# Performance work log

Hardware: AMD Instinct MI355X
Metric: run time of the kernel (lower is better)

The kernel has to match this reference:

```python
import jax, jax.numpy as jnp
import numpy as np

N = 50000      # nodes
E = 800000     # edges
F_IN = 128     # input_channels
H = 128        # hidden_channels
OUT = 10       # output_channels
G = 64         # graphs in batch


def setup_inputs() -> dict:
    key = jax.random.key(0)
    ks = jax.random.split(key, 16)
    s = 0.05
    inp = {
        "x": jax.random.normal(ks[0], (N, F_IN), jnp.float32),
        "edge_index": jax.random.randint(ks[1], (2, E), 0, N, jnp.int64 if jax.config.jax_enable_x64 else jnp.int32),
        "batch": jnp.sort(jax.random.randint(ks[2], (N,), 0, G, jnp.int32)),
        "conv1_w": jax.random.normal(ks[3], (F_IN, H), jnp.float32) * s,
        "conv1_b": jnp.zeros((H,), jnp.float32),
        "conv2_w": jax.random.normal(ks[4], (H, H), jnp.float32) * s,
        "conv2_b": jnp.zeros((H,), jnp.float32),
        "conv3_w": jax.random.normal(ks[5], (H, H), jnp.float32) * s,
        "conv3_b": jnp.zeros((H,), jnp.float32),
        "fc1_w": jax.random.normal(ks[6], (H, 8 * H), jnp.float32) * s,
        "fc1_b": jnp.zeros((8 * H,), jnp.float32),
        "fc2_w": jax.random.normal(ks[7], (8 * H, 4 * H), jnp.float32) * s,
        "fc2_b": jnp.zeros((4 * H,), jnp.float32),
        "fc3_w": jax.random.normal(ks[8], (4 * H, 2 * H), jnp.float32) * s,
        "fc3_b": jnp.zeros((2 * H,), jnp.float32),
        "fc4_w": jax.random.normal(ks[9], (2 * H, H), jnp.float32) * s,
        "fc4_b": jnp.zeros((H,), jnp.float32),
        "fc5_w": jax.random.normal(ks[10], (H, OUT), jnp.float32) * s,
        "fc5_b": jnp.zeros((OUT,), jnp.float32),
    }
    return inp


def _gcn_conv(x, w, b, src, dst, norm, n_nodes):
    # GCNConv: out = D^{-1/2} (A + I) D^{-1/2} X W + b   (self-loops already in src/dst)
    xw = x @ w                                        # [N, H]
    msg = xw[src] * norm[:, None]                     # gather + scale, [E+N, H]
    return jax.ops.segment_sum(msg, dst, num_segments=n_nodes) + b


def reference(x, edge_index, batch,
              conv1_w, conv1_b, conv2_w, conv2_b, conv3_w, conv3_b,
              fc1_w, fc1_b, fc2_w, fc2_b, fc3_w, fc3_b,
              fc4_w, fc4_b, fc5_w, fc5_b):
    n = x.shape[0]
    loop = jnp.arange(n, dtype=edge_index.dtype)
    src = jnp.concatenate([edge_index[0], loop])      # add self-loops
    dst = jnp.concatenate([edge_index[1], loop])
    deg = jax.ops.segment_sum(jnp.ones_like(dst, dtype=x.dtype), dst, num_segments=n)
    dinv = jnp.where(deg > 0, jax.lax.rsqrt(deg), 0.0)
    norm = dinv[src] * dinv[dst]                      # symmetric normalization per edge

    h = jax.nn.relu(_gcn_conv(x, conv1_w, conv1_b, src, dst, norm, n))
    h = jax.nn.relu(_gcn_conv(h, conv2_w, conv2_b, src, dst, norm, n))
    h = _gcn_conv(h, conv3_w, conv3_b, src, dst, norm, n)

    # global mean pool over graphs
    sums = jax.ops.segment_sum(h, batch, num_segments=G)
    cnt = jax.ops.segment_sum(jnp.ones((n,), x.dtype), batch, num_segments=G)
    f = sums / jnp.maximum(cnt, 1.0)[:, None]         # [G, H]

    y = jax.nn.relu(f @ fc1_w + fc1_b)
    y = jax.nn.relu(y @ fc2_w + fc2_b)
    y = jax.nn.relu(y @ fc3_w + fc3_b)
    y = jax.nn.relu(y @ fc4_w + fc4_b)
    # dropout p=0.5 is identity in eval mode
    y = y @ fc5_w + fc5_b                             # [G, OUT]
    return (f, y)
```

## Files before the change

### kernel.cpp

```cpp
#include <hip/hip_runtime.h>
#include <stdint.h>

#define N_NODES 50000
#define N_EDGES 800000
#define N_PAD   50176
#define PCHUNK  512
#define NCHUNKS 98
#define FEAT    128
#define NGRAPH  64

#define E_BLKS      3125
#define GSTRIP_BLKS 782
#define GR_BLKS     (GSTRIP_BLKS + E_BLKS)
#define CZ_BLKS     3136
#define CP_BLKS     1563
#define Z2_BLKS     65
#define PREP_BLKS   (32 + CZ_BLKS + CP_BLKS + Z2_BLKS)
#define E1_SPLIT    399872
#define AGGC_GRID   (1563 * 9)

typedef __attribute__((ext_vector_type(8))) short short8;
typedef __attribute__((ext_vector_type(4))) float floatx4;

static __device__ __forceinline__ ushort f2bf(float f) {
  uint32_t x = __float_as_uint(f);
  x += 0x7FFF + ((x >> 16) & 1);
  return (ushort)(x >> 16);
}
static __device__ __forceinline__ float bfLo(uint32_t u) {
  return __uint_as_float(u << 16);
}
static __device__ __forceinline__ float bfHi(uint32_t u) {
  return __uint_as_float(u & 0xFFFF0000u);
}

static __device__ __forceinline__ void cvt4T(const float* __restrict__ in,
                                             ushort* __restrict__ outT, int i) {
  float4 v = ((const float4*)in)[i];
  int k = (4 * i) >> 7;
  int n = (4 * i) & 127;
  outT[(size_t)(n + 0) * FEAT + k] = f2bf(v.x);
  outT[(size_t)(n + 1) * FEAT + k] = f2bf(v.y);
  outT[(size_t)(n + 2) * FEAT + k] = f2bf(v.z);
  outT[(size_t)(n + 3) * FEAT + k] = f2bf(v.w);
}

__global__ __launch_bounds__(256) void prep_fused(const float* __restrict__ w0,
                                                  const float* __restrict__ w1,
                                                  ushort* __restrict__ wbT,
                                                  float* __restrict__ coefT,
                                                  float4* __restrict__ zcnt,
                                                  float4* __restrict__ zfy) {
  int b = blockIdx.x, t = threadIdx.x;
  if (b < 32) {
    int i = b * 256 + t;
    if (i < 4096) cvt4T(w0, wbT, i);
    else cvt4T(w1, wbT + FEAT * FEAT, i - 4096);
  } else if (b < 32 + CZ_BLKS) {
    int i = (b - 32) * 256 + t;
    ((float4*)coefT)[i] = make_float4(0.f, 0.f, 0.f, 0.f);
  } else if (b < 32 + CZ_BLKS + CP_BLKS) {
    int i = (b - 32 - CZ_BLKS) * 256 + t;
    if (i < 400000) zcnt[i] = make_float4(0.f, 0.f, 0.f, 0.f);
  } else {
    int i = (b - 32 - CZ_BLKS - CP_BLKS) * 256 + t;
    if (i < 16400) zfy[i] = make_float4(0.f, 0.f, 0.f, 0.f);
  }
}

static __device__ __forceinline__ void gemm_strip_f32a(int strip, int lane,
                                                       const float* __restrict__ X,
                                                       const ushort* __restrict__ WT,
                                                       ushort* __restrict__ XW) {
  if (strip >= N_NODES / 16) return;
  int m0 = strip * 16;
  int r = lane & 15, quad = lane >> 4;
  const float* xrow = X + (size_t)(m0 + r) * FEAT;
  short8 afr[4];
#pragma unroll
  for (int kb = 0; kb < 4; ++kb) {
    int k0 = kb * 32 + quad * 8;
    float4 f0 = *(const float4*)(xrow + k0);
    float4 f1 = *(const float4*)(xrow + k0 + 4);
    short8 a;
    a[0] = (short)f2bf(f0.x); a[1] = (short)f2bf(f0.y);
    a[2] = (short)f2bf(f0.z); a[3] = (short)f2bf(f0.w);
    a[4] = (short)f2bf(f1.x); a[5] = (short)f2bf(f1.y);
    a[6] = (short)f2bf(f1.z); a[7] = (short)f2bf(f1.w);
    afr[kb] = a;
  }
#pragma unroll
  for (int nt = 0; nt < 8; ++nt) {
    int n0 = nt * 16;
    floatx4 acc = {0.f, 0.f, 0.f, 0.f};
    const ushort* wrow = WT + (size_t)(n0 + r) * FEAT;
#pragma unroll
    for (int kb = 0; kb < 4; ++kb) {
      short8 b = *(const short8*)(wrow + kb * 32 + quad * 8);
      acc = __builtin_amdgcn_mfma_f32_16x16x32_bf16(afr[kb], b, acc, 0, 0, 0);
    }
#pragma unroll
    for (int reg = 0; reg < 4; ++reg)
      XW[(size_t)(m0 + quad * 4 + reg) * FEAT + n0 + r] = f2bf(acc[reg]);
  }
}

__global__ __launch_bounds__(256) void gemm_rank(const float* __restrict__ x,
                                                 const ushort* __restrict__ wbT,
                                                 ushort* __restrict__ msl,
                                                 const int* __restrict__ dst,
                                                 int* __restrict__ cnt_p,
                                                 int* __restrict__ rank) {
  int b = blockIdx.x, t = threadIdx.x;
  int fifth = b / 5;
  if (b - fifth * 5 == 0) {
    gemm_strip_f32a(fifth * 4 + (t >> 6), t & 63, x, wbT, msl);
  } else {
    int e = (b - fifth - 1) * 256 + t;
    rank[e] = atomicAdd(&cnt_p[dst[e] * 32], 1);
  }
}

__global__ __launch_bounds__(256) void gemm2_strip(const ushort* __restrict__ X,
                                                   const ushort* __restrict__ WT,
                                                   ushort* __restrict__ XW) {
  int strip = (blockIdx.x * 256 + threadIdx.x) >> 6;
  int lane = threadIdx.x & 63;
  if (strip >= N_NODES / 16) return;
  int m0 = strip * 16;
  int r = lane & 15, quad = lane >> 4;
  const ushort* xrow = X + (size_t)(m0 + r) * FEAT;
  short8 afr[4];
#pragma unroll
  for (int kb = 0; kb < 4; ++kb)
    afr[kb] = *(const short8*)(xrow + kb * 32 + quad * 8);
#pragma unroll
  for (int nt = 0; nt < 8; ++nt) {
    int n0 = nt * 16;
    floatx4 acc = {0.f, 0.f, 0.f, 0.f};
    const ushort* wrow = WT + (size_t)(n0 + r) * FEAT;
#pragma unroll
    for (int kb = 0; kb < 4; ++kb) {
      short8 b = *(const short8*)(wrow + kb * 32 + quad * 8);
      acc = __builtin_amdgcn_mfma_f32_16x16x32_bf16(afr[kb], b, acc, 0, 0, 0);
    }
#pragma unroll
    for (int reg = 0; reg < 4; ++reg)
      XW[(size_t)(m0 + quad * 4 + reg) * FEAT + n0 + r] = f2bf(acc[reg]);
  }
}

__global__ __launch_bounds__(256) void dinv_scan1(const int* __restrict__ cnt_p,
                                                  const int* __restrict__ batch,
                                                  float* __restrict__ dinv,
                                                  float* __restrict__ cnt_g,
                                                  int* __restrict__ ptr,
                                                  int* __restrict__ bsums,
                                                  float* __restrict__ coefT) {
  __shared__ int tmp[256];
  __shared__ int bins[NGRAPH];
  if (threadIdx.x < NGRAPH) bins[threadIdx.x] = 0;
  int i = blockIdx.x * 256 + threadIdx.x;
  int v = (i < N_NODES) ? cnt_p[i * 32] : 0;
  tmp[threadIdx.x] = v;
  __syncthreads();
  for (int off = 1; off < 256; off <<= 1) {
    int t = (threadIdx.x >= off) ? tmp[threadIdx.x - off] : 0;
    __syncthreads();
    tmp[threadIdx.x] += t;
    __syncthreads();
  }
  if (i < N_NODES) ptr[i] = tmp[threadIdx.x] - v;
  if (threadIdx.x == 255) bsums[blockIdx.x] = tmp[255];
  if (i < N_NODES) {
    float di = rsqrtf((float)v + 1.0f);
    dinv[i] = di;
    int g = batch[i];
    coefT[(size_t)g * N_PAD + i] = di * di;
    atomicAdd(&bins[g], 1);
  }
  __syncthreads();
  if (threadIdx.x < NGRAPH && bins[threadIdx.x] > 0)
    atomicAdd(&cnt_g[threadIdx.x], (float)bins[threadIdx.x]);
}

__global__ __launch_bounds__(256) void scan2(int* __restrict__ bsums, int nb) {
  __shared__ int tmp[256];
  int v = (threadIdx.x < nb) ? bsums[threadIdx.x] : 0;
  tmp[threadIdx.x] = v;
  __syncthreads();
  for (int off = 1; off < 256; off <<= 1) {
    int t = (threadIdx.x >= off) ? tmp[threadIdx.x - off] : 0;
    __syncthreads();
    tmp[threadIdx.x] += t;
    __syncthreads();
  }
  if (threadIdx.x < nb) bsums[threadIdx.x] = tmp[threadIdx.x] - v;
}

__global__ __launch_bounds__(256) void fill_csr(const int* __restrict__ src,
                                                const int* __restrict__ dst,
                                                const int* __restrict__ rank,
                                                const int* __restrict__ ptr,
                                                const int* __restrict__ bsums,
                                                const float* __restrict__ dinv,
                                                int2* __restrict__ edges) {
  int e = blockIdx.x * 256 + threadIdx.x;
  if (e >= N_EDGES) return;
  int s = src[e];
  int d = dst[e];
  edges[ptr[d] + bsums[d >> 8] + rank[e]] = make_int2(s, __float_as_int(dinv[s]));
}

static __device__ __forceinline__ float2 agg_node(const uint32_t* __restrict__ m32,
                                                  const int2* __restrict__ edges,
                                                  int start, int n, int lane) {
  float ax0 = 0.f, ay0 = 0.f, ax1 = 0.f, ay1 = 0.f;
  float ax2 = 0.f, ay2 = 0.f, ax3 = 0.f, ay3 = 0.f;
  int i = 0;
  if ((start & 1) && n > 0) {
    int2 e = edges[start];
    uint32_t u = m32[(size_t)e.x * 64 + lane];
    float nrm = __int_as_float(e.y);
    ax0 = fmaf(nrm, bfLo(u), ax0);
    ay0 = fmaf(nrm, bfHi(u), ay0);
    i = 1;
  }
  for (; i + 16 <= n; i += 16) {
    const int4* ep = (const int4*)(edges + start + i);
    int4 q0 = ep[0], q1 = ep[1], q2 = ep[2], q3 = ep[3];
    int4 q4 = ep[4], q5 = ep[5], q6 = ep[6], q7 = ep[7];
    uint32_t u0 = m32[(size_t)q0.x * 64 + lane];
    uint32_t u1 = m32[(size_t)q0.z * 64 + lane];
    uint32_t u2 = m32[(size_t)q1.x * 64 + lane];
    uint32_t u3 = m32[(size_t)q1.z * 64 + lane];
    uint32_t u4 = m32[(size_t)q2.x * 64 + lane];
    uint32_t u5 = m32[(size_t)q2.z * 64 + lane];
    uint32_t u6 = m32[(size_t)q3.x * 64 + lane];
    uint32_t u7 = m32[(size_t)q3.z * 64 + lane];
    uint32_t u8 = m32[(size_t)q4.x * 64 + lane];
    uint32_t u9 = m32[(size_t)q4.z * 64 + lane];
    uint32_t uA = m32[(size_t)q5.x * 64 + lane];
    uint32_t uB = m32[(size_t)q5.z * 64 + lane];
    uint32_t uC = m32[(size_t)q6.x * 64 + lane];
    uint32_t uD = m32[(size_t)q6.z * 64 + lane];
    uint32_t uE = m32[(size_t)q7.x * 64 + lane];
    uint32_t uF = m32[(size_t)q7.z * 64 + lane];
    float n0 = __int_as_float(q0.y), n1 = __int_as_float(q0.w);
    float n2 = __int_as_float(q1.y), n3 = __int_as_float(q1.w);
    float n4 = __int_as_float(q2.y), n5 = __int_as_float(q2.w);
    float n6 = __int_as_float(q3.y), n7 = __int_as_float(q3.w);
    float n8 = __int_as_float(q4.y), n9 = __int_as_float(q4.w);
    float nA = __int_as_float(q5.y), nB = __int_as_float(q5.w);
    float nC = __int_as_float(q6.y), nD = __int_as_float(q6.w);
    float nE = __int_as_float(q7.y), nF = __int_as_float(q7.w);
    ax0 = fmaf(n0, bfLo(u0), ax0); ay0 = fmaf(n0, bfHi(u0), ay0);
    ax1 = fmaf(n1, bfLo(u1), ax1); ay1 = fmaf(n1, bfHi(u1), ay1);
    ax2 = fmaf(n2, bfLo(u2), ax2); ay2 = fmaf(n2, bfHi(u2), ay2);
    ax3 = fmaf(n3, bfLo(u3), ax3); ay3 = fmaf(n3, bfHi(u3), ay3);
    ax0 = fmaf(n4, bfLo(u4), ax0); ay0 = fmaf(n4, bfHi(u4), ay0);
    ax1 = fmaf(n5, bfLo(u5), ax1); ay1 = fmaf(n5, bfHi(u5), ay1);
    ax2 = fmaf(n6, bfLo(u6), ax2); ay2 = fmaf(n6, bfHi(u6), ay2);
    ax3 = fmaf(n7, bfLo(u7), ax3); ay3 = fmaf(n7, bfHi(u7), ay3);
    ax0 = fmaf(n8, bfLo(u8), ax0); ay0 = fmaf(n8, bfHi(u8), ay0);
    ax1 = fmaf(n9, bfLo(u9), ax1); ay1 = fmaf(n9, bfHi(u9), ay1);
    ax2 = fmaf(nA, bfLo(uA), ax2); ay2 = fmaf(nA, bfHi(uA), ay2);
    ax3 = fmaf(nB, bfLo(uB), ax3); ay3 = fmaf(nB, bfHi(uB), ay3);
    ax0 = fmaf(nC, bfLo(uC), ax0); ay0 = fmaf(nC, bfHi(uC), ay0);
    ax1 = fmaf(nD, bfLo(uD), ax1); ay1 = fmaf(nD, bfHi(uD), ay1);
    ax2 = fmaf(nE, bfLo(uE), ax2); ay2 = fmaf(nE, bfHi(uE), ay2);
    ax3 = fmaf(nF, bfLo(uF), ax3); ay3 = fmaf(nF, bfHi(uF), ay3);
  }
  if (i + 8 <= n) {
    const int4* ep = (const int4*)(edges + start + i);
    int4 q0 = ep[0], q1 = ep[1], q2 = ep[2], q3 = ep[3];
    uint32_t u0 = m32[(size_t)q0.x * 64 + lane];
    uint32_t u1 = m32[(size_t)q0.z * 64 + lane];
    uint32_t u2 = m32[(size_t)q1.x * 64 + lane];
    uint32_t u3 = m32[(size_t)q1.z * 64 + lane];
    uint32_t u4 = m32[(size_t)q2.x * 64 + lane];
    uint32_t u5 = m32[(size_t)q2.z * 64 + lane];
    uint32_t u6 = m32[(size_t)q3.x * 64 + lane];
    uint32_t u7 = m32[(size_t)q3.z * 64 + lane];
    float n0 = __int_as_float(q0.y), n1 = __int_as_float(q0.w);
    float n2 = __int_as_float(q1.y), n3 = __int_as_float(q1.w);
    float n4 = __int_as_float(q2.y), n5 = __int_as_float(q2.w);
    float n6 = __int_as_float(q3.y), n7 = __int_as_float(q3.w);
    ax0 = fmaf(n0, bfLo(u0), ax0); ay0 = fmaf(n0, bfHi(u0), ay0);
    ax1 = fmaf(n1, bfLo(u1), ax1); ay1 = fmaf(n1, bfHi(u1), ay1);
    ax2 = fmaf(n2, bfLo(u2), ax2); ay2 = fmaf(n2, bfHi(u2), ay2);
    ax3 = fmaf(n3, bfLo(u3), ax3); ay3 = fmaf(n3, bfHi(u3), ay3);
    ax0 = fmaf(n4, bfLo(u4), ax0); ay0 = fmaf(n4, bfHi(u4), ay0);
    ax1 = fmaf(n5, bfLo(u5), ax1); ay1 = fmaf(n5, bfHi(u5), ay1);
    ax2 = fmaf(n6, bfLo(u6), ax2); ay2 = fmaf(n6, bfHi(u6), ay2);
    ax3 = fmaf(n7, bfLo(u7), ax3); ay3 = fmaf(n7, bfHi(u7), ay3);
    i += 8;
  }
  if (i + 4 <= n) {
    const int4* ep = (const int4*)(edges + start + i);
    int4 q0 = ep[0], q1 = ep[1];
    uint32_t u0 = m32[(size_t)q0.x * 64 + lane];
    uint32_t u1 = m32[(size_t)q0.z * 64 + lane];
    uint32_t u2 = m32[(size_t)q1.x * 64 + lane];
    uint32_t u3 = m32[(size_t)q1.z * 64 + lane];
    float n0 = __int_as_float(q0.y), n1 = __int_as_float(q0.w);
    float n2 = __int_as_float(q1.y), n3 = __int_as_float(q1.w);
    ax0 = fmaf(n0, bfLo(u0), ax0); ay0 = fmaf(n0, bfHi(u0), ay0);
    ax1 = fmaf(n1, bfLo(u1), ax1); ay1 = fmaf(n1, bfHi(u1), ay1);
    ax2 = fmaf(n2, bfLo(u2), ax2); ay2 = fmaf(n2, bfHi(u2), ay2);
    ax3 = fmaf(n3, bfLo(u3), ax3); ay3 = fmaf(n3, bfHi(u3), ay3);
    i += 4;
  }
  if (i + 2 <= n) {
    const int4* ep = (const int4*)(edges + start + i);
    int4 q0 = ep[0];
    uint32_t u0 = m32[(size_t)q0.x * 64 + lane];
    uint32_t u1 = m32[(size_t)q0.z * 64 + lane];
    float n0 = __int_as_float(q0.y), n1 = __int_as_float(q0.w);
    ax0 = fmaf(n0, bfLo(u0), ax0); ay0 = fmaf(n0, bfHi(u0), ay0);
    ax1 = fmaf(n1, bfLo(u1), ax1); ay1 = fmaf(n1, bfHi(u1), ay1);
    i += 2;
  }
  for (; i < n; ++i) {
    int2 e = edges[start + i];
    float nrm = __int_as_float(e.y);
    uint32_t u = m32[(size_t)e.x * 64 + lane];
    ax0 = fmaf(nrm, bfLo(u), ax0);
    ay0 = fmaf(nrm, bfHi(u), ay0);
  }
  return make_float2((ax0 + ax1) + (ax2 + ax3), (ay0 + ay1) + (ay2 + ay3));
}

static __device__ __forceinline__ void agg_one(int v, int lane,
                                               const ushort* __restrict__ msg,
                                               const float* __restrict__ dinv,
                                               const int* __restrict__ ptr,
                                               const int* __restrict__ bsums,
                                               const int* __restrict__ cnt_p,
                                               const int2* __restrict__ edges,
                                               const float* __restrict__ bias,
                                               ushort* __restrict__ outp) {
  float di = dinv[v];
  const uint32_t* m32 = (const uint32_t*)msg;
  uint32_t su = m32[(size_t)v * 64 + lane];
  int start = ptr[v] + bsums[v >> 8];
  float2 s = agg_node(m32, edges, start, cnt_p[v * 32], lane);
  float ax = fmaf(fmaf(di, bfLo(su), s.x), di, bias[2 * lane]);
  float ay = fmaf(fmaf(di, bfHi(su), s.y), di, bias[2 * lane + 1]);
  ushort2 h2;
  h2.x = f2bf(fmaxf(ax, 0.f));
  h2.y = f2bf(fmaxf(ay, 0.f));
  ((ushort2*)outp)[(size_t)v * 64 + lane] = h2;
}

template <int PHASE>
__global__ __launch_bounds__(256) void agg_coef(const ushort* __restrict__ msg,
                                                const float* __restrict__ dinv,
                                                const int* __restrict__ ptr,
                                                const int* __restrict__ bsums,
                                                const int* __restrict__ cnt_p,
                                                const int2* __restrict__ edges,
                                                const float* __restrict__ bias,
                                                ushort* __restrict__ outp,
                                                const int* __restrict__ src,
                                                const int* __restrict__ dst,
                                                const int* __restrict__ batch,
                                                float* __restrict__ coefT) {
  int b = blockIdx.x, t = threadIdx.x;
  int grp = b / 9;
  int rem = b - grp * 9;
  if (rem < 8) {
    int ab = grp * 8 + rem;
    if (ab >= 12500) return;
    agg_one(ab * 4 + (t >> 6), t & 63, msg, dinv, ptr, bsums, cnt_p, edges,
            bias, outp);
  } else {
    int e = (PHASE ? E1_SPLIT : 0) + grp * 256 + t;
    if (e < (PHASE ? N_EDGES : E1_SPLIT)) {
      int s = src[e], d = dst[e];
      atomicAdd(&coefT[(size_t)batch[d] * N_PAD + s], dinv[s] * dinv[d]);
    }
  }
}

__global__ __launch_bounds__(512) void pool_mfma(const ushort* __restrict__ h2,
                                                 const float* __restrict__ coefT,
                                                 float* __restrict__ P) {
  __shared__ ushort cs[64 * PCHUNK];
  int t = threadIdx.x;
  int lane = t & 63;
  int w = t >> 6;
  int r = lane & 15, quad = lane >> 4;
  int n0 = w * 16;
  floatx4 acc[4];
#pragma unroll
  for (int mt = 0; mt < 4; ++mt) acc[mt] = (floatx4){0.f, 0.f, 0.f, 0.f};
#pragma unroll 1
  for (int cc = 0; cc < 2; ++cc) {
    int c0 = (blockIdx.x * 2 + cc) * PCHUNK;
#pragma unroll 4
    for (int it = 0; it < 16; ++it) {
      int f4 = t + it * 512;
      int g = f4 >> 7;
      int k = (f4 & 127) * 4;
      float4 v = *(const float4*)(coefT + (size_t)g * N_PAD + c0 + k);
      ushort4 u;
      u.x = f2bf(v.x); u.y = f2bf(v.y); u.z = f2bf(v.z); u.w = f2bf(v.w);
      uint32_t off = ((uint32_t)g * (PCHUNK * 2) + k * 2) ^ ((g & 7) << 4);
      *(ushort4*)((char*)cs + off) = u;
    }
    __syncthreads();
#pragma unroll 2
    for (int kb = 0; kb < 16; ++kb) {
      int k0c = kb * 32 + quad * 8;
      short8 bfr;
#pragma unroll
      for (int j = 0; j < 8; ++j)
        bfr[j] = (short)h2[(size_t)(c0 + k0c + j) * FEAT + n0 + r];
#pragma unroll
      for (int mt = 0; mt < 4; ++mt) {
        int row = mt * 16 + r;
        uint32_t off = ((uint32_t)row * (PCHUNK * 2) + k0c * 2) ^ ((row & 7) << 4);
        short8 a = *(const short8*)((const char*)cs + off);
        acc[mt] = __builtin_amdgcn_mfma_f32_16x16x32_bf16(a, bfr, acc[mt], 0, 0, 0);
      }
    }
    __syncthreads();
  }
#pragma unroll
  for (int mt = 0; mt < 4; ++mt)
#pragma unroll
    for (int reg = 0; reg < 4; ++reg)
      atomicAdd(&P[(size_t)(mt * 16 + quad * 4 + reg) * FEAT + n0 + r],
                acc[mt][reg]);
}

template <int K, int C, int KSLICE, int RELU_IN, int DIVC, int NSPLIT>
__global__ __launch_bounds__(256) void fc_layer(const float* __restrict__ IN,
                                                const float* __restrict__ W,
                                                const float* __restrict__ Bs,
                                                const float* __restrict__ cntg,
                                                float* __restrict__ OUT) {
  constexpr int CB = (C + 63) / 64;
  int lane = threadIdx.x & 63;
  int gq = threadIdx.x >> 6;
  int bid = blockIdx.x;
  int kp = bid % NSPLIT;
  int rest = bid / NSPLIT;
  int cg = rest % CB;
  int g = (rest / CB) * 4 + gq;
  int c = cg * 64 + lane;
  if (c >= C) return;
  int k0 = kp * KSLICE;
  const float* wp = W + (size_t)k0 * C + c;
  const float* in = IN + (size_t)g * K + k0;
  float cf = 1.f;
  if (DIVC) cf = fmaxf(cntg[g], 1.f);
  float a0 = 0.f, a1 = 0.f, a2 = 0.f, a3 = 0.f;
  float a4 = 0.f, a5 = 0.f, a6 = 0.f, a7 = 0.f;
#pragma unroll 2
  for (int k = 0; k < KSLICE; k += 8) {
    float i0 = in[k + 0], i1 = in[k + 1], i2 = in[k + 2], i3 = in[k + 3];
    float i4 = in[k + 4], i5 = in[k + 5], i6 = in[k + 6], i7 = in[k + 7];
    if (RELU_IN) {
      i0 = fmaxf(i0, 0.f); i1 = fmaxf(i1, 0.f);
      i2 = fmaxf(i2, 0.f); i3 = fmaxf(i3, 0.f);
      i4 = fmaxf(i4, 0.f); i5 = fmaxf(i5, 0.f);
      i6 = fmaxf(i6, 0.f); i7 = fmaxf(i7, 0.f);
    }
    if (DIVC) {
      i0 /= cf; i1 /= cf; i2 /= cf; i3 /= cf;
      i4 /= cf; i5 /= cf; i6 /= cf; i7 /= cf;
    }
    a0 = fmaf(i0, wp[(size_t)(k + 0) * C], a0);
    a1 = fmaf(i1, wp[(size_t)(k + 1) * C], a1);
    a2 = fmaf(i2, wp[(size_t)(k + 2) * C], a2);
    a3 = fmaf(i3, wp[(size_t)(k + 3) * C], a3);
    a4 = fmaf(i4, wp[(size_t)(k + 4) * C], a4);
    a5 = fmaf(i5, wp[(size_t)(k + 5) * C], a5);
    a6 = fmaf(i6, wp[(size_t)(k + 6) * C], a6);
    a7 = fmaf(i7, wp[(size_t)(k + 7) * C], a7);
  }
  float s = ((a0 + a1) + (a2 + a3)) + ((a4 + a5) + (a6 + a7));
  if (NSPLIT == 1) {
    OUT[(size_t)g * C + c] = s + Bs[c];
  } else {
    atomicAdd(&OUT[(size_t)g * C + c], s + (kp == 0 ? Bs[c] : 0.f));
  }
}

extern "C" void kernel_launch(void* const* d_in, const int* in_sizes, int n_in,
                              void* d_out, int out_size, void* d_ws, size_t ws_size,
                              hipStream_t stream) {
  const float* x         = (const float*)d_in[0];
  const int*   ei        = (const int*)d_in[1];
  const int*   batch     = (const int*)d_in[2];
  const float* conv_w[3] = {(const float*)d_in[3], (const float*)d_in[5], (const float*)d_in[7]};
  const float* conv_b[3] = {(const float*)d_in[4], (const float*)d_in[6], (const float*)d_in[8]};
  const float* fc_w[5]   = {(const float*)d_in[9],  (const float*)d_in[11],
                            (const float*)d_in[13], (const float*)d_in[15],
                            (const float*)d_in[17]};
  const float* fc_b[5]   = {(const float*)d_in[10], (const float*)d_in[12],
                            (const float*)d_in[14], (const float*)d_in[16],
                            (const float*)d_in[18]};
  const int* e_src = ei;
  const int* e_dst = ei + N_EDGES;
  float* out_f = (float*)d_out;
  float* out_y = (float*)d_out + NGRAPH * FEAT;

  char* p = (char*)d_ws;
  auto carve = [&](size_t bytes) {
    char* r = p;
    p += (bytes + 255) & ~(size_t)255;
    return r;
  };
  int*    cnt_p   = (int*)carve((size_t)N_NODES * 128);
  float*  dinv    = (float*)carve(N_NODES * 4);
  int*    csr_ptr = (int*)carve(N_NODES * 4);
  int*    bsums   = (int*)carve(256 * 4);
  int2*   edges   = (int2*)carve((size_t)N_EDGES * 8);
  ushort* wbT     = (ushort*)carve((size_t)2 * FEAT * FEAT * 2);
  ushort* hbuf    = (ushort*)carve((size_t)N_PAD * FEAT * 2);
  float*  coefT   = (float*)carve((size_t)NGRAPH * N_PAD * 4);
  float*  f_sum   = (float*)carve(NGRAPH * FEAT * 4);
  float*  cnt_g   = (float*)carve(NGRAPH * 4);
  float*  Y2      = (float*)carve(NGRAPH * 512 * 4);
  float*  Y3      = (float*)carve(NGRAPH * 256 * 4);
  float*  Y4      = (float*)carve(NGRAPH * 128 * 4);
  float*  Y1      = (float*)carve(NGRAPH * 1024 * 4);
  char*   region  = carve((size_t)N_EDGES * 4 + (size_t)N_NODES * FEAT * 2);
  int*    rank    = (int*)region;
  ushort* msl1    = (ushort*)(region + (size_t)N_EDGES * 4);
  ushort* msl2    = (ushort*)region;

  const int BLK_N = (N_NODES + 255) / 256;

  prep_fused<<<PREP_BLKS, 256, 0, stream>>>(conv_w[0], conv_w[1], wbT, coefT,
                                            (float4*)cnt_p, (float4*)f_sum);

  gemm_rank<<<GR_BLKS, 256, 0, stream>>>(x, wbT, msl1, e_dst, cnt_p, rank);

  dinv_scan1<<<BLK_N, 256, 0, stream>>>(cnt_p, batch, dinv, cnt_g, csr_ptr,
                                        bsums, coefT);
  scan2<<<1, 256, 0, stream>>>(bsums, BLK_N);

  fill_csr<<<E_BLKS, 256, 0, stream>>>(e_src, e_dst, rank, csr_ptr, bsums,
                                       dinv, edges);

  agg_coef<0><<<AGGC_GRID, 256, 0, stream>>>(
      msl1, dinv, csr_ptr, bsums, cnt_p, edges, conv_b[0], hbuf,
      e_src, e_dst, batch, coefT);
  gemm2_strip<<<GSTRIP_BLKS, 256, 0, stream>>>(hbuf, wbT + FEAT * FEAT, msl2);
  agg_coef<1><<<AGGC_GRID, 256, 0, stream>>>(
      msl2, dinv, csr_ptr, bsums, cnt_p, edges, conv_b[1], hbuf,
      e_src, e_dst, batch, coefT);
  pool_mfma<<<NCHUNKS / 2, 512, 0, stream>>>(hbuf, coefT, f_sum);

  fc_layer< 128, 128, 128, 0, 1, 1><<< 32, 256, 0, stream>>>(f_sum, conv_w[2], conv_b[2], cnt_g, out_f);
  fc_layer< 128,1024, 128, 0, 0, 1><<<256, 256, 0, stream>>>(out_f, fc_w[0], fc_b[0], nullptr, Y1);
  fc_layer<1024, 512, 256, 1, 0, 4><<<512, 256, 0, stream>>>(Y1, fc_w[1], fc_b[1], nullptr, Y2);
  fc_layer< 512, 256, 128, 1, 0, 4><<<256, 256, 0, stream>>>(Y2, fc_w[2], fc_b[2], nullptr, Y3);
  fc_layer< 256, 128,  32, 1, 0, 8><<<256, 256, 0, stream>>>(Y3, fc_w[3], fc_b[3], nullptr, Y4);
  fc_layer< 128,  10, 128, 1, 0, 1><<< 16, 256, 0, stream>>>(Y4, fc_w[4], fc_b[4], nullptr, out_y);
}
```

Baseline: 331.5 us.

## Fold scan2 into dinv_scan1 via last-block ticket and move coef atomics into CSR aggregation

Removes the separate single-block scan2 launch by having the last block to finish dinv_scan1 (found through an atomic ticket) scan the block sums. The coefficient-matrix atomics previously came from a separate edge-parallel slice of each aggregation launch, split across both layers. They are now done entirely inside the first aggregation pass, reading the already-built CSR edges (src index and dinv[src]) per destination node. This drops the reloads of src/dst/batch/dinv per edge and simplifies the grid, but makes the first aggregation carry all the atomic work. The ticket relies on a counter that is zeroed by the prep kernel's enlarged zero range.

```diff
diff --git a/kernel.cpp b/kernel.cpp
--- a/kernel.cpp
+++ b/kernel.cpp
@@ -14,10 +14,10 @@
 #define GR_BLKS     (GSTRIP_BLKS + E_BLKS)
 #define CZ_BLKS     3136
 #define CP_BLKS     1563
+#define Z2_F4       16416
 #define Z2_BLKS     65
 #define PREP_BLKS   (32 + CZ_BLKS + CP_BLKS + Z2_BLKS)
-#define E1_SPLIT    399872
-#define AGGC_GRID   (1563 * 9)
+#define AGG_BLKS    12500
 
 typedef __attribute__((ext_vector_type(8))) short short8;
 typedef __attribute__((ext_vector_type(4))) float floatx4;
@@ -64,7 +64,7 @@
     if (i < 400000) zcnt[i] = make_float4(0.f, 0.f, 0.f, 0.f);
   } else {
     int i = (b - 32 - CZ_BLKS - CP_BLKS) * 256 + t;
-    if (i < 16400) zfy[i] = make_float4(0.f, 0.f, 0.f, 0.f);
+    if (i < Z2_F4) zfy[i] = make_float4(0.f, 0.f, 0.f, 0.f);
   }
 }
 
@@ -156,9 +156,11 @@
                                                   float* __restrict__ cnt_g,
                                                   int* __restrict__ ptr,
                                                   int* __restrict__ bsums,
-                                                  float* __restrict__ coefT) {
+                                                  float* __restrict__ coefT,
+                                                  int* __restrict__ ticket) {
   __shared__ int tmp[256];
   __shared__ int bins[NGRAPH];
+  __shared__ int lastFlag;
   if (threadIdx.x < NGRAPH) bins[threadIdx.x] = 0;
   int i = blockIdx.x * 256 + threadIdx.x;
   int v = (i < N_NODES) ? cnt_p[i * 32] : 0;
@@ -171,7 +173,11 @@
     __syncthreads();
   }
   if (i < N_NODES) ptr[i] = tmp[threadIdx.x] - v;
-  if (threadIdx.x == 255) bsums[blockIdx.x] = tmp[255];
+  if (threadIdx.x == 255) {
+    bsums[blockIdx.x] = tmp[255];
+    __threadfence();
+    lastFlag = (atomicAdd(ticket, 1) == (int)gridDim.x - 1);
+  }
   if (i < N_NODES) {
     float di = rsqrtf((float)v + 1.0f);
     dinv[i] = di;
@@ -182,20 +188,20 @@
   __syncthreads();
   if (threadIdx.x < NGRAPH && bins[threadIdx.x] > 0)
     atomicAdd(&cnt_g[threadIdx.x], (float)bins[threadIdx.x]);
-}
-
-__global__ __launch_bounds__(256) void scan2(int* __restrict__ bsums, int nb) {
-  __shared__ int tmp[256];
-  int v = (threadIdx.x < nb) ? bsums[threadIdx.x] : 0;
-  tmp[threadIdx.x] = v;
   __syncthreads();
-  for (int off = 1; off < 256; off <<= 1) {
-    int t = (threadIdx.x >= off) ? tmp[threadIdx.x - off] : 0;
+  if (lastFlag) {
+    __threadfence();
+    int b = (threadIdx.x < (int)gridDim.x) ? bsums[threadIdx.x] : 0;
+    tmp[threadIdx.x] = b;
     __syncthreads();
-    tmp[threadIdx.x] += t;
-    __syncthreads();
-  }
-  if (threadIdx.x < nb) bsums[threadIdx.x] = tmp[threadIdx.x] - v;
+    for (int off = 1; off < 256; off <<= 1) {
+      int t = (threadIdx.x >= off) ? tmp[threadIdx.x - off] : 0;
+      __syncthreads();
+      tmp[threadIdx.x] += t;
+      __syncthreads();
+    }
+    if (threadIdx.x < (int)gridDim.x) bsums[threadIdx.x] = tmp[threadIdx.x] - b;
+  }
 }
 
 __global__ __launch_bounds__(256) void fill_csr(const int* __restrict__ src,
@@ -331,30 +337,8 @@
   return make_float2((ax0 + ax1) + (ax2 + ax3), (ay0 + ay1) + (ay2 + ay3));
 }
 
-static __device__ __forceinline__ void agg_one(int v, int lane,
-                                               const ushort* __restrict__ msg,
-                                               const float* __restrict__ dinv,
-                                               const int* __restrict__ ptr,
-                                               const int* __restrict__ bsums,
-                                               const int* __restrict__ cnt_p,
-                                               const int2* __restrict__ edges,
-                                               const float* __restrict__ bias,
-                                               ushort* __restrict__ outp) {
-  float di = dinv[v];
-  const uint32_t* m32 = (const uint32_t*)msg;
-  uint32_t su = m32[(size_t)v * 64 + lane];
-  int start = ptr[v] + bsums[v >> 8];
-  float2 s = agg_node(m32, edges, start, cnt_p[v * 32], lane);
-  float ax = fmaf(fmaf(di, bfLo(su), s.x), di, bias[2 * lane]);
-  float ay = fmaf(fmaf(di, bfHi(su), s.y), di, bias[2 * lane + 1]);
-  ushort2 h2;
-  h2.x = f2bf(fmaxf(ax, 0.f));
-  h2.y = f2bf(fmaxf(ay, 0.f));
-  ((ushort2*)outp)[(size_t)v * 64 + lane] = h2;
-}
-
-template <int PHASE>
-__global__ __launch_bounds__(256) void agg_coef(const ushort* __restrict__ msg,
+template <int DO_COEF>
+__global__ __launch_bounds__(256) void agg_pass(const ushort* __restrict__ msg,
                                                 const float* __restrict__ dinv,
                                                 const int* __restrict__ ptr,
                                                 const int* __restrict__ bsums,
@@ -362,25 +346,31 @@
                                                 const int2* __restrict__ edges,
                                                 const float* __restrict__ bias,
                                                 ushort* __restrict__ outp,
-                                                const int* __restrict__ src,
-                                                const int* __restrict__ dst,
                                                 const int* __restrict__ batch,
                                                 float* __restrict__ coefT) {
-  int b = blockIdx.x, t = threadIdx.x;
-  int grp = b / 9;
-  int rem = b - grp * 9;
-  if (rem < 8) {
-    int ab = grp * 8 + rem;
-    if (ab >= 12500) return;
-    agg_one(ab * 4 + (t >> 6), t & 63, msg, dinv, ptr, bsums, cnt_p, edges,
-            bias, outp);
-  } else {
-    int e = (PHASE ? E1_SPLIT : 0) + grp * 256 + t;
-    if (e < (PHASE ? N_EDGES : E1_SPLIT)) {
-      int s = src[e], d = dst[e];
-      atomicAdd(&coefT[(size_t)batch[d] * N_PAD + s], dinv[s] * dinv[d]);
-    }
-  }
+  int wave = (blockIdx.x * 256 + threadIdx.x) >> 6;
+  int lane = threadIdx.x & 63;
+  if (wave >= N_NODES) return;
+  int v = wave;
+  float di = dinv[v];
+  const uint32_t* m32 = (const uint32_t*)msg;
+  uint32_t su = m32[(size_t)v * 64 + lane];
+  int start = ptr[v] + bsums[v >> 8];
+  int n = cnt_p[v * 32];
+  float2 s = agg_node(m32, edges, start, n, lane);
+  if (DO_COEF) {
+    size_t grow = (size_t)batch[v] * N_PAD;
+    for (int j = lane; j < n; j += 64) {
+      int2 e = edges[start + j];
+      atomicAdd(&coefT[grow + e.x], __int_as_float(e.y) * di);
+    }
+  }
+  float ax = fmaf(fmaf(di, bfLo(su), s.x), di, bias[2 * lane]);
+  float ay = fmaf(fmaf(di, bfHi(su), s.y), di, bias[2 * lane + 1]);
+  ushort2 h2;
+  h2.x = f2bf(fmaxf(ax, 0.f));
+  h2.y = f2bf(fmaxf(ay, 0.f));
+  ((ushort2*)outp)[(size_t)v * 64 + lane] = h2;
 }
 
 __global__ __launch_bounds__(512) void pool_mfma(const ushort* __restrict__ h2,
@@ -524,6 +514,7 @@
   float*  coefT   = (float*)carve((size_t)NGRAPH * N_PAD * 4);
   float*  f_sum   = (float*)carve(NGRAPH * FEAT * 4);
   float*  cnt_g   = (float*)carve(NGRAPH * 4);
+  int*    ticket  = (int*)carve(256);
   float*  Y2      = (float*)carve(NGRAPH * 512 * 4);
   float*  Y3      = (float*)carve(NGRAPH * 256 * 4);
   float*  Y4      = (float*)carve(NGRAPH * 128 * 4);
@@ -541,19 +532,16 @@
   gemm_rank<<<GR_BLKS, 256, 0, stream>>>(x, wbT, msl1, e_dst, cnt_p, rank);
 
   dinv_scan1<<<BLK_N, 256, 0, stream>>>(cnt_p, batch, dinv, cnt_g, csr_ptr,
-                                        bsums, coefT);
-  scan2<<<1, 256, 0, stream>>>(bsums, BLK_N);
+                                        bsums, coefT, ticket);
 
   fill_csr<<<E_BLKS, 256, 0, stream>>>(e_src, e_dst, rank, csr_ptr, bsums,
                                        dinv, edges);
 
-  agg_coef<0><<<AGGC_GRID, 256, 0, stream>>>(
-      msl1, dinv, csr_ptr, bsums, cnt_p, edges, conv_b[0], hbuf,
-      e_src, e_dst, batch, coefT);
+  agg_pass<1><<<AGG_BLKS, 256, 0, stream>>>(msl1, dinv, csr_ptr, bsums, cnt_p,
+                                            edges, conv_b[0], hbuf, batch, coefT);
   gemm2_strip<<<GSTRIP_BLKS, 256, 0, stream>>>(hbuf, wbT + FEAT * FEAT, msl2);
-  agg_coef<1><<<AGGC_GRID, 256, 0, stream>>>(
-      msl2, dinv, csr_ptr, bsums, cnt_p, edges, conv_b[1], hbuf,
-      e_src, e_dst, batch, coefT);
+  agg_pass<0><<<AGG_BLKS, 256, 0, stream>>>(msl2, dinv, csr_ptr, bsums, cnt_p,
+                                            edges, conv_b[1], hbuf, batch, coefT);
   pool_mfma<<<NCHUNKS / 2, 512, 0, stream>>>(hbuf, coefT, f_sum);
 
   fc_layer< 128, 128, 128, 0, 1, 1><<< 32, 256, 0, stream>>>(f_sum, conv_w[2], conv_b[2], cnt_g, out_f);
```

Measured after the change: 340.8 us. 2.8% more time.
